# Performance work log

Measured on AMD Instinct MI355X. Metric: run time of the kernel, lower is better.

The kernel has to match this reference:

```python
import jax, jax.numpy as jnp
import numpy as np

U, DP, TOPK, NH = 2, 16, 8, 2
D = 512
M = DP ** U          # 256 slots
DK = U * DP          # 32 addressing dim
BETA_MAX = 2.0


def setup_inputs():
    key = jax.random.key(0)
    ks = jax.random.split(key, 12)
    B, T = 8, 128
    s = 0.02
    return {
        "h": jax.random.normal(ks[0], (B, T, D), jnp.float32),
        "K_slots": jax.random.normal(ks[1], (B, M, D), jnp.float32) * s,
        "V_slots": jax.random.normal(ks[2], (B, M, D), jnp.float32) * s,
        "z_K": jnp.ones((B, M), jnp.float32),
        "z_V": jnp.ones((B, M), jnp.float32),
        "W_k": jax.random.normal(ks[3], (DK, D), jnp.float32) * s,
        "W_q": jax.random.normal(ks[4], (DK, D), jnp.float32) * s,
        "log_tau_w": jnp.zeros((1,), jnp.float32),
        "log_tau_r": jnp.zeros((1,), jnp.float32),
        "hh_k": jax.random.normal(ks[5], (NH, D, D), jnp.float32) * s,
        "hh_vk": jax.random.normal(ks[6], (NH, D, D), jnp.float32) * s,
        "hh_vv": jax.random.normal(ks[7], (NH, D, D), jnp.float32) * s,
        "hh_bw": jax.random.normal(ks[8], (NH, 1, D), jnp.float32) * s,
        "hh_bb": jnp.zeros((NH, 1), jnp.float32),
        "gamma": jnp.float32(1.0),
        "W_out": jax.random.normal(ks[9], (D, D), jnp.float32) * s,
        "W_gate": jax.random.normal(ks[10], (D, D), jnp.float32) * s,
    }


def _kron_address(z, log_tau):
    # z: [B, DK]; Kronecker-factored softmax address over M = DP**U slots
    B = z.shape[0]
    probs = jax.nn.softmax(z.reshape(B, U, DP) / jnp.exp(log_tau[0]), axis=-1)
    addr = probs[:, 0]
    for u in range(1, U):
        addr = (addr[:, :, None] * probs[:, u, None, :]).reshape(B, -1)
    w, idx = jax.lax.top_k(addr, TOPK)
    return idx, w


def _forward(h, K_slots, V_slots, z_K, z_V, W_k, W_q, log_tau_w, log_tau_r,
             hh_k, hh_vk, hh_vv, hh_bw, hh_bb, gamma, W_out, W_gate,
             checkpoint=False):
    B, T, _ = h.shape
    scale = D ** -0.5
    b_idx = jnp.arange(B)[:, None]
    sp_gamma = jax.nn.softplus(gamma)

    def step(carry, h_t):
        K_s, V_s, zK, zV = carry
        write_idx, write_w = _kron_address(h_t @ W_k.T, log_tau_w)
        read_idx, _ = _kron_address(h_t @ W_q.T, log_tau_r)
        # scatter write weights into dense [B, M] (top-k indices are unique)
        w_full = jnp.zeros((B, M), h_t.dtype).at[b_idx, write_idx].set(write_w)
        # PDMA decay
        decay = (1.0 - w_full) ** sp_gamma
        K_s = decay[..., None] * K_s
        V_s = decay[..., None] * V_s
        zK = decay * zK + w_full
        zV = decay * zV + w_full
        # gather active slots: [B, K, D]
        K_act = jnp.take_along_axis(K_s, write_idx[:, :, None], axis=1)
        V_act = jnp.take_along_axis(V_s, write_idx[:, :, None], axis=1)
        # Householder update chain
        for j in range(NH):
            k_j = jax.nn.silu(h_t @ hh_k[j].T)
            k_hat = k_j / jnp.maximum(
                jnp.linalg.norm(k_j, axis=-1, keepdims=True), 1e-12)
            v_kj = h_t @ hh_vk[j].T
            v_vj = h_t @ hh_vv[j].T
            beta = BETA_MAX * jax.nn.sigmoid(h_t @ hh_bw[j].T + hh_bb[j])  # [B,1]
            kh = k_hat[:, None, :]
            be = beta[:, None, :]
            K_act = K_act - be * kh * (kh * K_act).sum(-1, keepdims=True) \
                    + be * k_j[:, None, :] * v_kj[:, None, :]
            V_act = V_act - be * kh * (kh * V_act).sum(-1, keepdims=True) \
                    + be * k_j[:, None, :] * v_vj[:, None, :]
        # scatter updated slots back
        K_s = K_s.at[b_idx, write_idx].set(K_act)
        V_s = V_s.at[b_idx, write_idx].set(V_act)
        # read path
        K_read = jnp.take_along_axis(K_s, read_idx[:, :, None], axis=1)
        V_read = jnp.take_along_axis(V_s, read_idx[:, :, None], axis=1)
        zK_read = jnp.take_along_axis(zK, read_idx, axis=1)[..., None]
        zV_read = jnp.take_along_axis(zV, read_idx, axis=1)[..., None]
        K_n = K_read / zK_read
        V_n = V_read / zV_read
        rel = (K_n * h_t[:, None, :]).sum(-1)           # [B, K]
        attn = jax.nn.softmax(rel * scale, axis=-1)
        readout = (attn[..., None] * V_n).sum(1)        # [B, D]
        out = jax.nn.sigmoid(h_t @ W_gate.T) * (readout @ W_out.T)
        return (K_s, V_s, zK, zV), (out, write_idx, read_idx)

    step_fn = jax.checkpoint(step) if checkpoint else step
    (K_s, V_s, zK, zV), (outs, widx, ridx) = jax.lax.scan(
        step_fn, (K_slots, V_slots, z_K, z_V), jnp.swapaxes(h, 0, 1))
    return (jnp.swapaxes(outs, 0, 1), K_s, V_s, zK, zV, widx[-1], ridx[-1])


def reference(h, K_slots, V_slots, z_K, z_V, W_k, W_q, log_tau_w, log_tau_r,
              hh_k, hh_vk, hh_vv, hh_bw, hh_bb, gamma, W_out, W_gate):
    return _forward(h, K_slots, V_slots, z_K, z_V, W_k, W_q, log_tau_w,
                    log_tau_r, hh_k, hh_vk, hh_vv, hh_bw, hh_bb, gamma,
                    W_out, W_gate)
```

## Files before the change

### kernel.cpp

```cpp
#include <hip/hip_runtime.h>
#include <math.h>

#define D_ 512
#define M_ 256
#define T_ 128
#define B_ 8
#define TOPK_ 8
#define NH_ 2
#define BT_ (B_*T_)

__device__ __forceinline__ float wred(float v){
#pragma unroll
  for (int m = 1; m < 64; m <<= 1) v += __shfl_xor(v, m, 64);
  return v;
}
__device__ __forceinline__ float4 ld4(const float* p){ return *(const float4*)p; }
__device__ __forceinline__ void st4(float* p, float4 v){ *(float4*)p = v; }
__device__ __forceinline__ float dot4(float4 a, float4 b){
  return a.x*b.x + a.y*b.y + a.z*b.z + a.w*b.w;
}
__device__ __forceinline__ float4 scl4(float4 a, float s){
  a.x*=s; a.y*=s; a.z*=s; a.w*=s; return a;
}

template<int CTRL>
__device__ __forceinline__ float dpp_add(float x){
  int y = __builtin_amdgcn_update_dpp(0, __float_as_int(x), CTRL, 0xf, 0xf, true);
  return x + __int_as_float(y);
}
__device__ __forceinline__ float wredd(float x){
  x = dpp_add<0x111>(x);
  x = dpp_add<0x112>(x);
  x = dpp_add<0x114>(x);
  x = dpp_add<0x118>(x);
  x = dpp_add<0x142>(x);
  x = dpp_add<0x143>(x);
  return __int_as_float(__builtin_amdgcn_readlane(__float_as_int(x), 63));
}

__device__ __forceinline__ void bar_lgkm(){
  asm volatile("s_waitcnt lgkmcnt(0)\n\ts_barrier" ::: "memory");
}

__global__ __launch_bounds__(64) void addr_kernel(
    const float* __restrict__ h, const float* __restrict__ Wk,
    const float* __restrict__ Wq, const float* __restrict__ ltw,
    const float* __restrict__ ltr, const float* __restrict__ gammap,
    float* __restrict__ metab)
{
  const int bt = blockIdx.x;
  const int tid = threadIdx.x;
  __shared__ float p_s[64];

  const float* hrow = h + (size_t)bt*D_;
  const float* wrow = (tid < 32) ? (Wk + (size_t)tid*D_)
                                 : (Wq + (size_t)(tid-32)*D_);
  float dot = 0.f;
  for (int d = 0; d < D_; d += 4){
    float4 hv = ld4(&hrow[d]); float4 wv = ld4(&wrow[d]);
    dot += hv.x*wv.x + hv.y*wv.y + hv.z*wv.z + hv.w*wv.w;
  }
  float tau = (tid < 32) ? expf(ltw[0]) : expf(ltr[0]);
  float mx = dot;
#pragma unroll
  for (int m = 1; m < 16; m <<= 1) mx = fmaxf(mx, __shfl_xor(mx, m, 64));
  float e = expf((dot - mx)/tau);
  float sm = e;
#pragma unroll
  for (int m = 1; m < 16; m <<= 1) sm += __shfl_xor(sm, m, 64);
  p_s[tid] = e / sm;
  __syncthreads();

  const int half = tid >> 5;
  const int l = tid & 31;
  const int g0 = half*32, g1 = half*32 + 16;
  float av[8];
#pragma unroll
  for (int k = 0; k < 8; ++k){
    int x = l*8 + k;
    av[k] = p_s[g0 + (x>>4)] * p_s[g1 + (x&15)];
  }
  const float sp = log1pf(expf(gammap[0]));
  for (int r = 0; r < TOPK_; ++r){
    float bv = -1.f; int bi = 0;
#pragma unroll
    for (int k = 0; k < 8; ++k){ if (av[k] > bv){ bv = av[k]; bi = l*8+k; } }
#pragma unroll
    for (int m = 1; m < 32; m <<= 1){
      float ov = __shfl_xor(bv, m, 64); int oi = __shfl_xor(bi, m, 64);
      if (ov > bv || (ov == bv && oi < bi)){ bv = ov; bi = oi; }
    }
    if ((bi >> 3) == l) av[bi & 7] = -2.f;
    float* mp = metab + (size_t)(bt*TOPK_ + r)*4;
    if (tid == 0){
      mp[0] = __int_as_float(bi); mp[1] = bv; mp[2] = powf(1.f - bv, sp);
    }
    if (tid == 32) mp[3] = __int_as_float(bi);
  }
}

struct GemmPtrs { const float* W[6]; float* C[6]; };

__global__ __launch_bounds__(256) void gemm_nt(
    const float* __restrict__ A, GemmPtrs p)
{
  const float* W = p.W[blockIdx.z];
  float* C = p.C[blockIdx.z];
  const int n0 = blockIdx.x * 64;
  const int m0 = blockIdx.y * 64;
  const int tid = threadIdx.x;
  __shared__ __align__(16) float As[16][68];
  __shared__ __align__(16) float Bs[16][68];
  const int r  = tid >> 2;
  const int c4 = (tid & 3) << 2;
  const int tx4 = (tid & 15) << 2;
  const int ty4 = (tid >> 4) << 2;
  float acc[4][4] = {{0.f}};

  for (int kc = 0; kc < 512; kc += 16){
    float4 av = ld4(&A[(size_t)(m0+r)*512 + kc + c4]);
    float4 wv = ld4(&W[(size_t)(n0+r)*512 + kc + c4]);
    __syncthreads();
    As[c4+0][r]=av.x; As[c4+1][r]=av.y; As[c4+2][r]=av.z; As[c4+3][r]=av.w;
    Bs[c4+0][r]=wv.x; Bs[c4+1][r]=wv.y; Bs[c4+2][r]=wv.z; Bs[c4+3][r]=wv.w;
    __syncthreads();
#pragma unroll
    for (int k = 0; k < 16; ++k){
      float4 a  = ld4(&As[k][ty4]);
      float4 bq = ld4(&Bs[k][tx4]);
      acc[0][0]+=a.x*bq.x; acc[0][1]+=a.x*bq.y; acc[0][2]+=a.x*bq.z; acc[0][3]+=a.x*bq.w;
      acc[1][0]+=a.y*bq.x; acc[1][1]+=a.y*bq.y; acc[1][2]+=a.y*bq.z; acc[1][3]+=a.y*bq.w;
      acc[2][0]+=a.z*bq.x; acc[2][1]+=a.z*bq.y; acc[2][2]+=a.z*bq.z; acc[2][3]+=a.z*bq.w;
      acc[3][0]+=a.w*bq.x; acc[3][1]+=a.w*bq.y; acc[3][2]+=a.w*bq.z; acc[3][3]+=a.w*bq.w;
    }
  }
#pragma unroll
  for (int i = 0; i < 4; ++i){
    float4 cv; cv.x=acc[i][0]; cv.y=acc[i][1]; cv.z=acc[i][2]; cv.w=acc[i][3];
    st4(&C[(size_t)(m0+ty4+i)*512 + n0 + tx4], cv);
  }
}

__global__ __launch_bounds__(256) void gemm_out(
    const float* __restrict__ h, const float* __restrict__ rdo,
    const float* __restrict__ Wg, const float* __restrict__ Wo,
    float* __restrict__ C)
{
  const int n0 = blockIdx.x * 64;
  const int m0 = blockIdx.y * 64;
  const int tid = threadIdx.x;
  __shared__ __align__(16) float Ag[16][68];
  __shared__ __align__(16) float Ao[16][68];
  __shared__ __align__(16) float Bg[16][68];
  __shared__ __align__(16) float Bo[16][68];
  const int r  = tid >> 2;
  const int c4 = (tid & 3) << 2;
  const int tx4 = (tid & 15) << 2;
  const int ty4 = (tid >> 4) << 2;
  float accg[4][4] = {{0.f}};
  float acco[4][4] = {{0.f}};

  for (int kc = 0; kc < 512; kc += 16){
    float4 a1 = ld4(&h  [(size_t)(m0+r)*512 + kc + c4]);
    float4 a2 = ld4(&rdo[(size_t)(m0+r)*512 + kc + c4]);
    float4 w1 = ld4(&Wg [(size_t)(n0+r)*512 + kc + c4]);
    float4 w2 = ld4(&Wo [(size_t)(n0+r)*512 + kc + c4]);
    __syncthreads();
    Ag[c4+0][r]=a1.x; Ag[c4+1][r]=a1.y; Ag[c4+2][r]=a1.z; Ag[c4+3][r]=a1.w;
    Ao[c4+0][r]=a2.x; Ao[c4+1][r]=a2.y; Ao[c4+2][r]=a2.z; Ao[c4+3][r]=a2.w;
    Bg[c4+0][r]=w1.x; Bg[c4+1][r]=w1.y; Bg[c4+2][r]=w1.z; Bg[c4+3][r]=w1.w;
    Bo[c4+0][r]=w2.x; Bo[c4+1][r]=w2.y; Bo[c4+2][r]=w2.z; Bo[c4+3][r]=w2.w;
    __syncthreads();
#pragma unroll
    for (int k = 0; k < 16; ++k){
      float4 ag = ld4(&Ag[k][ty4]);
      float4 ao = ld4(&Ao[k][ty4]);
      float4 bg = ld4(&Bg[k][tx4]);
      float4 bo = ld4(&Bo[k][tx4]);
      accg[0][0]+=ag.x*bg.x; accg[0][1]+=ag.x*bg.y; accg[0][2]+=ag.x*bg.z; accg[0][3]+=ag.x*bg.w;
      accg[1][0]+=ag.y*bg.x; accg[1][1]+=ag.y*bg.y; accg[1][2]+=ag.y*bg.z; accg[1][3]+=ag.y*bg.w;
      accg[2][0]+=ag.z*bg.x; accg[2][1]+=ag.z*bg.y; accg[2][2]+=ag.z*bg.z; accg[2][3]+=ag.z*bg.w;
      accg[3][0]+=ag.w*bg.x; accg[3][1]+=ag.w*bg.y; accg[3][2]+=ag.w*bg.z; accg[3][3]+=ag.w*bg.w;
      acco[0][0]+=ao.x*bo.x; acco[0][1]+=ao.x*bo.y; acco[0][2]+=ao.x*bo.z; acco[0][3]+=ao.x*bo.w;
      acco[1][0]+=ao.y*bo.x; acco[1][1]+=ao.y*bo.y; acco[1][2]+=ao.y*bo.z; acco[1][3]+=ao.y*bo.w;
      acco[2][0]+=ao.z*bo.x; acco[2][1]+=ao.z*bo.y; acco[2][2]+=ao.z*bo.z; acco[2][3]+=ao.z*bo.w;
      acco[3][0]+=ao.w*bo.x; acco[3][1]+=ao.w*bo.y; acco[3][2]+=ao.w*bo.z; acco[3][3]+=ao.w*bo.w;
    }
  }
#pragma unroll
  for (int i = 0; i < 4; ++i){
    float4 cv;
    cv.x = acco[i][0] / (1.f + expf(-accg[i][0]));
    cv.y = acco[i][1] / (1.f + expf(-accg[i][1]));
    cv.z = acco[i][2] / (1.f + expf(-accg[i][2]));
    cv.w = acco[i][3] / (1.f + expf(-accg[i][3]));
    st4(&C[(size_t)(m0+ty4+i)*512 + n0 + tx4], cv);
  }
}

__global__ __launch_bounds__(256) void ew2_kernel(
    float* __restrict__ khat, float* __restrict__ kvk, float* __restrict__ kvv,
    float* __restrict__ pre2, const float* __restrict__ h,
    const float* __restrict__ hh_bw, const float* __restrict__ hh_bb)
{
  const int bt = blockIdx.x;
  const int tid = threadIdx.x;
  const int wid = tid >> 6, lane = tid & 63;
  float* k0p  = khat + (size_t)bt*D_;
  float* k1p  = khat + (size_t)BT_*D_ + (size_t)bt*D_;
  float* vk0p = kvk  + (size_t)bt*D_;
  float* vk1p = kvk  + (size_t)BT_*D_ + (size_t)bt*D_;
  float* vv0p = kvv  + (size_t)bt*D_;
  float* vv1p = kvv  + (size_t)BT_*D_ + (size_t)bt*D_;
  const float* hp  = h + (size_t)bt*D_;

  float s0[2], s1[2];
  float n0 = 0.f, n1 = 0.f, bd0 = 0.f, bd1 = 0.f;
#pragma unroll
  for (int q = 0; q < 2; ++q){
    int d = tid + q*256;
    float x0 = k0p[d], x1 = k1p[d], hv = hp[d];
    float v0 = x0 / (1.f + expf(-x0));
    float v1 = x1 / (1.f + expf(-x1));
    s0[q] = v0; s1[q] = v1;
    n0 += v0*v0; n1 += v1*v1;
    bd0 += hv*hh_bw[d]; bd1 += hv*hh_bw[D_ + d];
  }
  __shared__ float4 rb[4];
  float4 acc = make_float4(wred(n0), wred(n1), wred(bd0), wred(bd1));
  if (lane == 0) rb[wid] = acc;
  __syncthreads();
  float4 t0 = rb[0], t1 = rb[1], t2 = rb[2], t3 = rb[3];
  n0 = t0.x+t1.x+t2.x+t3.x; n1 = t0.y+t1.y+t2.y+t3.y;
  bd0 = t0.z+t1.z+t2.z+t3.z; bd1 = t0.w+t1.w+t2.w+t3.w;
  float inv0 = 1.f / fmaxf(sqrtf(n0), 1e-12f);
  float inv1 = 1.f / fmaxf(sqrtf(n1), 1e-12f);
  float be0 = 2.f / (1.f + expf(-(bd0 + hh_bb[0])));
  float be1 = 2.f / (1.f + expf(-(bd1 + hh_bb[1])));

  float c01 = 0.f, dK = 0.f, dV = 0.f;
#pragma unroll
  for (int q = 0; q < 2; ++q){
    int d = tid + q*256;
    float kh0 = s0[q]*inv0, kh1 = s1[q]*inv1;
    float u0K = s0[q]*vk0p[d], u1K = s1[q]*vk1p[d];
    float u0V = s0[q]*vv0p[d], u1V = s1[q]*vv1p[d];
    k0p[d] = kh0; k1p[d] = kh1;
    vk0p[d] = be0*u0K + be1*u1K;
    vv0p[d] = be0*u0V + be1*u1V;
    c01 += kh1*kh0; dK += kh1*u0K; dV += kh1*u0V;
  }
  __syncthreads();
  float4 acc2 = make_float4(wred(c01), wred(dK), wred(dV), 0.f);
  if (lane == 0) rb[wid] = acc2;
  __syncthreads();
  if (tid == 0){
    float4 a = rb[0], b = rb[1], c = rb[2], d = rb[3];
    pre2[(size_t)bt*8+0] = a.x+b.x+c.x+d.x;
    pre2[(size_t)bt*8+1] = a.y+b.y+c.y+d.y;
    pre2[(size_t)bt*8+2] = a.z+b.z+c.z+d.z;
    pre2[(size_t)bt*8+3] = be0;
    pre2[(size_t)bt*8+4] = be1;
  }
}

__global__ __launch_bounds__(512, 2) void scan_kernel(
    float* __restrict__ Ks, float* __restrict__ Vs,
    const float* __restrict__ zK0, const float* __restrict__ zV0,
    const float* __restrict__ khat, const float* __restrict__ ucKb,
    const float* __restrict__ ucVb, const float* __restrict__ pre2,
    const float* __restrict__ metab, const float* __restrict__ h,
    float* __restrict__ readout,
    float* __restrict__ o_zK, float* __restrict__ o_zV,
    float* __restrict__ o_widx, float* __restrict__ o_ridx)
{
  __shared__ __align__(16) float ring[3][4*D_];
  __shared__ __align__(16) float fwdK[TOPK_][D_];
  __shared__ __align__(16) float fwdV[TOPK_][D_];
  __shared__ __align__(16) float Vr_s[TOPK_][D_];
  __shared__ float zK_s[M_], zV_s[M_];
  __shared__ float2 rel2_s[TOPK_];

  const int b = blockIdx.x;
  const int tid = threadIdx.x;
  const int s = tid >> 6, lane = tid & 63;
  const int l4 = lane * 4;
  const float scale = 0.044194173824159216f;

  float* Ksb = Ks + (size_t)b*M_*D_;
  float* Vsb = Vs + (size_t)b*M_*D_;
  const float* vbt[4] = { khat, khat + (size_t)BT_*D_, ucKb, ucVb };
  const float* srcc = vbt[s >> 1];
  const int goff = (s & 1)*256 + l4;
  const int loff = (s >> 1)*D_ + goff;
  const float4* mb = (const float4*)metab;

  const int bt0 = b*T_;
  for (int tt = 0; tt < 2; ++tt)
    st4(&ring[tt][loff], ld4(srcc + (size_t)(bt0+tt)*D_ + goff));
  float4 g = ld4(srcc + (size_t)(bt0+2)*D_ + goff);

  float4 me   = mb[bt0*TOPK_ + s];
  float4 me8  = mb[bt0*TOPK_ + (lane & 7)];
  int   mi  = __float_as_int(me.x);  float ww  = me.y;  float dec = me.z;
  int   ri  = __float_as_int(me.w);
  int   wv8 = __float_as_int(me8.x); int rv8 = __float_as_int(me8.w);
  float4 pm = *(const float4*)&pre2[(size_t)bt0*8];
  float be1v = pre2[(size_t)bt0*8+4];
  float c01 = pm.x, dKp = pm.y, dVp = pm.z, be0 = pm.w;

  const int bt1 = bt0 + 1;
  float4 me_n  = mb[bt1*TOPK_ + s];
  float4 me8_n = mb[bt1*TOPK_ + (lane & 7)];
  int   mi_n  = __float_as_int(me_n.x);  float ww_n = me_n.y;
  float dec_n = me_n.z;                  int ri_n  = __float_as_int(me_n.w);
  int   wv8_n = __float_as_int(me8_n.x); int rv8_n = __float_as_int(me8_n.w);
  float4 pm_n = *(const float4*)&pre2[(size_t)bt1*8];
  float be1_n = pre2[(size_t)bt1*8+4];

  float4 K0 = ld4(&Ksb[(size_t)mi*D_ + l4]);
  float4 K1 = ld4(&Ksb[(size_t)mi*D_ + 256 + l4]);
  float4 V0 = ld4(&Vsb[(size_t)mi*D_ + l4]);
  float4 V1 = ld4(&Vsb[(size_t)mi*D_ + 256 + l4]);
  float4 RK0 = ld4(&Ksb[(size_t)ri*D_ + l4]);
  float4 RK1 = ld4(&Ksb[(size_t)ri*D_ + 256 + l4]);
  float4 RV0 = ld4(&Vsb[(size_t)ri*D_ + l4]);
  float4 RV1 = ld4(&Vsb[(size_t)ri*D_ + 256 + l4]);

  if (tid < M_){ zK_s[tid] = zK0[b*M_+tid]; zV_s[tid] = zV0[b*M_+tid]; }
  __syncthreads();

  for (int t = 0; t < T_; ++t){
    const int bt = b*T_ + t;
    const float* rbuf = ring[t % 3];

    float4 HTa = ld4(h + (size_t)bt*D_ + l4);
    float4 HTb = ld4(h + (size_t)bt*D_ + 256 + l4);

    float4 kh0a = ld4(&rbuf[l4]),        kh0b = ld4(&rbuf[256+l4]);
    float4 kh1a = ld4(&rbuf[D_+l4]),     kh1b = ld4(&rbuf[D_+256+l4]);
    float4 ucKa = ld4(&rbuf[2*D_+l4]),   ucKb2 = ld4(&rbuf[2*D_+256+l4]);
    float4 ucVa = ld4(&rbuf[3*D_+l4]),   ucVb2 = ld4(&rbuf[3*D_+256+l4]);

    if (t > 0){
      float2 rz[TOPK_];
#pragma unroll
      for (int i = 0; i < TOPK_; ++i) rz[i] = rel2_s[i];
      float mx = rz[0].x;
#pragma unroll
      for (int i = 1; i < TOPK_; ++i) mx = fmaxf(mx, rz[i].x);
      float smm = 0.f, r = 0.f;
#pragma unroll
      for (int i = 0; i < TOPK_; ++i){
        float ev = __expf(rz[i].x - mx); smm += ev;
        r += ev * rz[i].y * Vr_s[i][tid];
      }
      readout[(size_t)(bt-1)*D_ + tid] = r / smm;
    }

    K0 = scl4(K0,dec); K1 = scl4(K1,dec);
    V0 = scl4(V0,dec); V1 = scl4(V1,dec);
    float aK = wredd(dot4(K0,kh0a) + dot4(K1,kh0b));
    float bK = wredd(dot4(K0,kh1a) + dot4(K1,kh1b));
    float aV = wredd(dot4(V0,kh0a) + dot4(V1,kh0b));
    float bV = wredd(dot4(V0,kh1a) + dot4(V1,kh1b));
    float p0K = be0*aK, p1K = be1v*(bK + be0*(dKp - aK*c01));
    float p0V = be0*aV, p1V = be1v*(bV + be0*(dVp - aV*c01));
    K0.x += ucKa.x  - p0K*kh0a.x - p1K*kh1a.x;
    K0.y += ucKa.y  - p0K*kh0a.y - p1K*kh1a.y;
    K0.z += ucKa.z  - p0K*kh0a.z - p1K*kh1a.z;
    K0.w += ucKa.w  - p0K*kh0a.w - p1K*kh1a.w;
    K1.x += ucKb2.x - p0K*kh0b.x - p1K*kh1b.x;
    K1.y += ucKb2.y - p0K*kh0b.y - p1K*kh1b.y;
    K1.z += ucKb2.z - p0K*kh0b.z - p1K*kh1b.z;
    K1.w += ucKb2.w - p0K*kh0b.w - p1K*kh1b.w;
    V0.x += ucVa.x  - p0V*kh0a.x - p1V*kh1a.x;
    V0.y += ucVa.y  - p0V*kh0a.y - p1V*kh1a.y;
    V0.z += ucVa.z  - p0V*kh0a.z - p1V*kh1a.z;
    V0.w += ucVa.w  - p0V*kh0a.w - p1V*kh1a.w;
    V1.x += ucVb2.x - p0V*kh0b.x - p1V*kh1b.x;
    V1.y += ucVb2.y - p0V*kh0b.y - p1V*kh1b.y;
    V1.z += ucVb2.z - p0V*kh0b.z - p1V*kh1b.z;
    V1.w += ucVb2.w - p0V*kh0b.w - p1V*kh1b.w;

    unsigned long long nf =
        __ballot((lane < 8) && (rv8   == mi)) |
        __ballot((lane < 8) && (wv8_n == mi)) |
        __ballot((lane < 8) && (rv8_n == mi));
    if (nf){
      st4(&fwdK[s][l4], K0); st4(&fwdK[s][256+l4], K1);
      st4(&fwdV[s][l4], V0); st4(&fwdV[s][256+l4], V1);
    }
    st4(&Ksb[(size_t)mi*D_ + l4], K0); st4(&Ksb[(size_t)mi*D_ + 256 + l4], K1);
    st4(&Vsb[(size_t)mi*D_ + l4], V0); st4(&Vsb[(size_t)mi*D_ + 256 + l4], V1);
    if (lane == 0)      zK_s[mi] = dec*zK_s[mi] + ww;
    else if (lane == 1) zV_s[mi] = dec*zV_s[mi] + ww;

    bar_lgkm();

    st4(&ring[(t+2)%3][loff], g);
    const int bt3 = (t+3 < T_) ? bt+3 : b*T_+T_-1;
    g = ld4(srcc + (size_t)bt3*D_ + goff);

    unsigned long long hS = __ballot((lane < 8) && (wv8 == mi_n));
    float4 nK0, nK1, nV0, nV1;
    if (hS){
      int w = __ffsll(hS) - 1;
      nK0 = ld4(&fwdK[w][l4]); nK1 = ld4(&fwdK[w][256+l4]);
      nV0 = ld4(&fwdV[w][l4]); nV1 = ld4(&fwdV[w][256+l4]);
    } else {
      nK0 = ld4(&Ksb[(size_t)mi_n*D_ + l4]);
      nK1 = ld4(&Ksb[(size_t)mi_n*D_ + 256 + l4]);
      nV0 = ld4(&Vsb[(size_t)mi_n*D_ + l4]);
      nV1 = ld4(&Vsb[(size_t)mi_n*D_ + 256 + l4]);
    }
    unsigned long long hR = __ballot((lane < 8) && (wv8 == ri_n));
    float4 nRK0, nRK1, nRV0, nRV1;
    if (hR){
      int w = __ffsll(hR) - 1;
      nRK0 = ld4(&fwdK[w][l4]); nRK1 = ld4(&fwdK[w][256+l4]);
      nRV0 = ld4(&fwdV[w][l4]); nRV1 = ld4(&fwdV[w][256+l4]);
    } else {
      nRK0 = ld4(&Ksb[(size_t)ri_n*D_ + l4]);
      nRK1 = ld4(&Ksb[(size_t)ri_n*D_ + 256 + l4]);
      nRV0 = ld4(&Vsb[(size_t)ri_n*D_ + l4]);
      nRV1 = ld4(&Vsb[(size_t)ri_n*D_ + 256 + l4]);
    }

    const int btnn = (t+2 < T_) ? bt+2 : b*T_+T_-1;
    float4 me_nn  = mb[btnn*TOPK_ + s];
    float4 me8_nn = mb[btnn*TOPK_ + (lane & 7)];
    float4 pm_nn  = *(const float4*)&pre2[(size_t)btnn*8];
    float  be1_nn = pre2[(size_t)btnn*8+4];

    unsigned long long mk = __ballot((lane < 8) && (wv8 == ri));
    float4 rk0, rk1, rv0, rv1;
    if (mk){
      int fm = __ffsll(mk) - 1;
      rk0 = ld4(&fwdK[fm][l4]); rk1 = ld4(&fwdK[fm][256+l4]);
      rv0 = ld4(&fwdV[fm][l4]); rv1 = ld4(&fwdV[fm][256+l4]);
    } else {
      rk0 = RK0; rk1 = RK1; rv0 = RV0; rv1 = RV1;
    }
    float dt = wredd(dot4(rk0,HTa) + dot4(rk1,HTb));
    st4(&Vr_s[s][l4], rv0); st4(&Vr_s[s][256+l4], rv1);
    if (lane == 0)
      rel2_s[s] = make_float2(dt * scale / zK_s[ri], 1.0f / zV_s[ri]);

    __syncthreads();

    K0=nK0; K1=nK1; V0=nV0; V1=nV1;
    RK0=nRK0; RK1=nRK1; RV0=nRV0; RV1=nRV1;
    mi=mi_n; ww=ww_n; dec=dec_n; ri=ri_n; wv8=wv8_n; rv8=rv8_n;
    c01=pm_n.x; dKp=pm_n.y; dVp=pm_n.z; be0=pm_n.w; be1v=be1_n;
    mi_n=__float_as_int(me_nn.x); ww_n=me_nn.y; dec_n=me_nn.z;
    ri_n=__float_as_int(me_nn.w);
    wv8_n=__float_as_int(me8_nn.x); rv8_n=__float_as_int(me8_nn.w);
    pm_n=pm_nn; be1_n=be1_nn;
  }

  {
    const int btL = b*T_ + T_ - 1;
    float2 rz[TOPK_];
#pragma unroll
    for (int i = 0; i < TOPK_; ++i) rz[i] = rel2_s[i];
    float mx = rz[0].x;
#pragma unroll
    for (int i = 1; i < TOPK_; ++i) mx = fmaxf(mx, rz[i].x);
    float smm = 0.f, r = 0.f;
#pragma unroll
    for (int i = 0; i < TOPK_; ++i){
      float ev = __expf(rz[i].x - mx); smm += ev;
      r += ev * rz[i].y * Vr_s[i][tid];
    }
    readout[(size_t)btL*D_ + tid] = r / smm;

    if (tid < M_){ o_zK[b*M_+tid] = zK_s[tid]; o_zV[b*M_+tid] = zV_s[tid]; }
    if (tid < TOPK_){
      float4 m = mb[btL*TOPK_ + tid];
      o_widx[b*TOPK_+tid] = (float)__float_as_int(m.x);
      o_ridx[b*TOPK_+tid] = (float)__float_as_int(m.w);
    }
  }
}

extern "C" void kernel_launch(void* const* d_in, const int* in_sizes, int n_in,
                              void* d_out, int out_size, void* d_ws, size_t ws_size,
                              hipStream_t stream)
{
  (void)in_sizes; (void)n_in; (void)out_size; (void)ws_size;
  const float* h       = (const float*)d_in[0];
  const float* K_slots = (const float*)d_in[1];
  const float* V_slots = (const float*)d_in[2];
  const float* z_K     = (const float*)d_in[3];
  const float* z_V     = (const float*)d_in[4];
  const float* W_k     = (const float*)d_in[5];
  const float* W_q     = (const float*)d_in[6];
  const float* ltw     = (const float*)d_in[7];
  const float* ltr     = (const float*)d_in[8];
  const float* hh_k    = (const float*)d_in[9];
  const float* hh_vk   = (const float*)d_in[10];
  const float* hh_vv   = (const float*)d_in[11];
  const float* hh_bw   = (const float*)d_in[12];
  const float* hh_bb   = (const float*)d_in[13];
  const float* gamma   = (const float*)d_in[14];
  const float* W_out   = (const float*)d_in[15];
  const float* W_gate  = (const float*)d_in[16];

  float* out    = (float*)d_out;
  float* o_outs = out;
  float* o_Ks   = out + 524288;
  float* o_Vs   = out + 1572864;
  float* o_zK   = out + 2621440;
  float* o_zV   = out + 2623488;
  float* o_widx = out + 2625536;
  float* o_ridx = out + 2625600;

  float* ws    = (float*)d_ws;
  float* khat  = ws;
  float* kvk   = ws + 2*(size_t)BT_*D_;
  float* kvv   = kvk + 2*(size_t)BT_*D_;
  float* rdo   = kvv + 2*(size_t)BT_*D_;
  float* metab = rdo + (size_t)BT_*D_;
  float* pre2  = metab + (size_t)BT_*TOPK_*4;

  (void)hipMemcpyAsync(o_Ks, K_slots, sizeof(float)*(size_t)B_*M_*D_,
                       hipMemcpyDeviceToDevice, stream);
  (void)hipMemcpyAsync(o_Vs, V_slots, sizeof(float)*(size_t)B_*M_*D_,
                       hipMemcpyDeviceToDevice, stream);

  addr_kernel<<<BT_, 64, 0, stream>>>(h, W_k, W_q, ltw, ltr, gamma, metab);

  GemmPtrs p{};
  p.W[0] = hh_k;           p.C[0] = khat;
  p.W[1] = hh_k + 262144;  p.C[1] = khat + (size_t)BT_*D_;
  p.W[2] = hh_vk;          p.C[2] = kvk;
  p.W[3] = hh_vk + 262144; p.C[3] = kvk + (size_t)BT_*D_;
  p.W[4] = hh_vv;          p.C[4] = kvv;
  p.W[5] = hh_vv + 262144; p.C[5] = kvv + (size_t)BT_*D_;
  gemm_nt<<<dim3(8,16,6), 256, 0, stream>>>(h, p);

  ew2_kernel<<<BT_, 256, 0, stream>>>(khat, kvk, kvv, pre2, h, hh_bw, hh_bb);

  scan_kernel<<<B_, 512, 0, stream>>>(o_Ks, o_Vs, z_K, z_V, khat, kvk, kvv,
                                      pre2, metab, h, rdo,
                                      o_zK, o_zV, o_widx, o_ridx);

  gemm_out<<<dim3(8,16), 256, 0, stream>>>(h, rdo, W_gate, W_out, o_outs);
}
```

Baseline: 510.5 us.

## Precompute slot normalizers in separate scan and simplify serial memory-update loop

The zK/zV normalizer recurrence moves into a new per-batch kernel that emits the reciprocal normalizers for each read index, so the main scan no longer keeps them in shared memory. The main scan drops the shared-memory forwarding of freshly written slots and instead re-reads slots from global memory after a barrier. Readout buffers are double-buffered so the softmax readout of the previous step can sit after the barrier. This removes ballot/forwarding logic and z bookkeeping from the serial critical path, at the cost of an extra kernel launch and global-memory read-after-write latency each step. It also relies on block-wide barriers making the global stores visible to the following loads.

```diff
diff --git a/kernel.cpp b/kernel.cpp
--- a/kernel.cpp
+++ b/kernel.cpp
@@ -38,10 +38,6 @@
   return __int_as_float(__builtin_amdgcn_readlane(__float_as_int(x), 63));
 }
 
-__device__ __forceinline__ void bar_lgkm(){
-  asm volatile("s_waitcnt lgkmcnt(0)\n\ts_barrier" ::: "memory");
-}
-
 __global__ __launch_bounds__(64) void addr_kernel(
     const float* __restrict__ h, const float* __restrict__ Wk,
     const float* __restrict__ Wq, const float* __restrict__ ltw,
@@ -97,6 +93,35 @@
     }
     if (tid == 32) mp[3] = __int_as_float(bi);
   }
+}
+
+__global__ __launch_bounds__(256) void zscan_kernel(
+    const float* __restrict__ zK0, const float* __restrict__ zV0,
+    const float* __restrict__ metab, float2* __restrict__ zr,
+    float* __restrict__ o_zK, float* __restrict__ o_zV)
+{
+  __shared__ __align__(16) float4 meta_s[T_*TOPK_];
+  const int b = blockIdx.x;
+  const int m = threadIdx.x;
+  const float4* mb = (const float4*)metab + (size_t)b*T_*TOPK_;
+#pragma unroll
+  for (int q = 0; q < 4; ++q) meta_s[m + q*256] = mb[m + q*256];
+  float zk = zK0[b*M_+m], zv = zV0[b*M_+m];
+  __syncthreads();
+  for (int t = 0; t < T_; ++t){
+#pragma unroll
+    for (int i = 0; i < TOPK_; ++i){
+      float4 me = meta_s[t*TOPK_+i];
+      if (m == __float_as_int(me.x)){ zk = me.z*zk + me.y; zv = me.z*zv + me.y; }
+    }
+#pragma unroll
+    for (int i = 0; i < TOPK_; ++i){
+      float4 me = meta_s[t*TOPK_+i];
+      if (m == __float_as_int(me.w))
+        zr[(size_t)(b*T_+t)*TOPK_+i] = make_float2(1.f/zk, 1.f/zv);
+    }
+  }
+  o_zK[b*M_+m] = zk; o_zV[b*M_+m] = zv;
 }
 
 struct GemmPtrs { const float* W[6]; float* C[6]; };
@@ -264,22 +289,17 @@
   }
 }
 
-__global__ __launch_bounds__(512, 2) void scan_kernel(
+__global__ __launch_bounds__(512) void scan_kernel(
     float* __restrict__ Ks, float* __restrict__ Vs,
-    const float* __restrict__ zK0, const float* __restrict__ zV0,
     const float* __restrict__ khat, const float* __restrict__ ucKb,
     const float* __restrict__ ucVb, const float* __restrict__ pre2,
-    const float* __restrict__ metab, const float* __restrict__ h,
-    float* __restrict__ readout,
-    float* __restrict__ o_zK, float* __restrict__ o_zV,
+    const float* __restrict__ metab, const float2* __restrict__ zr,
+    const float* __restrict__ h, float* __restrict__ readout,
     float* __restrict__ o_widx, float* __restrict__ o_ridx)
 {
-  __shared__ __align__(16) float ring[3][4*D_];
-  __shared__ __align__(16) float fwdK[TOPK_][D_];
-  __shared__ __align__(16) float fwdV[TOPK_][D_];
-  __shared__ __align__(16) float Vr_s[TOPK_][D_];
-  __shared__ float zK_s[M_], zV_s[M_];
-  __shared__ float2 rel2_s[TOPK_];
+  __shared__ __align__(16) float ring[4][4*D_];
+  __shared__ __align__(16) float Vr_s[2][TOPK_][D_];
+  __shared__ float2 rel2_s[2][TOPK_];
 
   const int b = blockIdx.x;
   const int tid = threadIdx.x;
@@ -296,67 +316,42 @@
   const float4* mb = (const float4*)metab;
 
   const int bt0 = b*T_;
-  for (int tt = 0; tt < 2; ++tt)
-    st4(&ring[tt][loff], ld4(srcc + (size_t)(bt0+tt)*D_ + goff));
+  st4(&ring[0][loff], ld4(srcc + (size_t)bt0*D_ + goff));
+  st4(&ring[1][loff], ld4(srcc + (size_t)(bt0+1)*D_ + goff));
   float4 g = ld4(srcc + (size_t)(bt0+2)*D_ + goff);
 
   float4 me   = mb[bt0*TOPK_ + s];
-  float4 me8  = mb[bt0*TOPK_ + (lane & 7)];
-  int   mi  = __float_as_int(me.x);  float ww  = me.y;  float dec = me.z;
-  int   ri  = __float_as_int(me.w);
-  int   wv8 = __float_as_int(me8.x); int rv8 = __float_as_int(me8.w);
-  float4 pm = *(const float4*)&pre2[(size_t)bt0*8];
-  float be1v = pre2[(size_t)bt0*8+4];
-  float c01 = pm.x, dKp = pm.y, dVp = pm.z, be0 = pm.w;
-
-  const int bt1 = bt0 + 1;
-  float4 me_n  = mb[bt1*TOPK_ + s];
-  float4 me8_n = mb[bt1*TOPK_ + (lane & 7)];
-  int   mi_n  = __float_as_int(me_n.x);  float ww_n = me_n.y;
-  float dec_n = me_n.z;                  int ri_n  = __float_as_int(me_n.w);
-  int   wv8_n = __float_as_int(me8_n.x); int rv8_n = __float_as_int(me8_n.w);
-  float4 pm_n = *(const float4*)&pre2[(size_t)bt1*8];
-  float be1_n = pre2[(size_t)bt1*8+4];
-
+  float4 me_n = mb[(bt0+1)*TOPK_ + s];
+  float4 pm   = ld4(&pre2[(size_t)bt0*8]);
+  float  be1v = pre2[(size_t)bt0*8+4];
+  float4 pm_n = ld4(&pre2[(size_t)(bt0+1)*8]);
+  float  be1_n= pre2[(size_t)(bt0+1)*8+4];
+  float2 zr2   = zr[(size_t)bt0*TOPK_ + s];
+  float2 zr2_n = zr[(size_t)(bt0+1)*TOPK_ + s];
+
+  int mi = __float_as_int(me.x);
   float4 K0 = ld4(&Ksb[(size_t)mi*D_ + l4]);
   float4 K1 = ld4(&Ksb[(size_t)mi*D_ + 256 + l4]);
   float4 V0 = ld4(&Vsb[(size_t)mi*D_ + l4]);
   float4 V1 = ld4(&Vsb[(size_t)mi*D_ + 256 + l4]);
-  float4 RK0 = ld4(&Ksb[(size_t)ri*D_ + l4]);
-  float4 RK1 = ld4(&Ksb[(size_t)ri*D_ + 256 + l4]);
-  float4 RV0 = ld4(&Vsb[(size_t)ri*D_ + l4]);
-  float4 RV1 = ld4(&Vsb[(size_t)ri*D_ + 256 + l4]);
-
-  if (tid < M_){ zK_s[tid] = zK0[b*M_+tid]; zV_s[tid] = zV0[b*M_+tid]; }
-  __syncthreads();
-
+  __syncthreads();
+
+#pragma unroll 4
   for (int t = 0; t < T_; ++t){
     const int bt = b*T_ + t;
-    const float* rbuf = ring[t % 3];
-
+    const float dec = me.z;
+    const int   ri  = __float_as_int(me.w);
+    mi = __float_as_int(me.x);
+
+    st4(&ring[(t+2)&3][loff], g);
     float4 HTa = ld4(h + (size_t)bt*D_ + l4);
     float4 HTb = ld4(h + (size_t)bt*D_ + 256 + l4);
 
+    const float* rbuf = ring[t & 3];
     float4 kh0a = ld4(&rbuf[l4]),        kh0b = ld4(&rbuf[256+l4]);
     float4 kh1a = ld4(&rbuf[D_+l4]),     kh1b = ld4(&rbuf[D_+256+l4]);
     float4 ucKa = ld4(&rbuf[2*D_+l4]),   ucKb2 = ld4(&rbuf[2*D_+256+l4]);
     float4 ucVa = ld4(&rbuf[3*D_+l4]),   ucVb2 = ld4(&rbuf[3*D_+256+l4]);
-
-    if (t > 0){
-      float2 rz[TOPK_];
-#pragma unroll
-      for (int i = 0; i < TOPK_; ++i) rz[i] = rel2_s[i];
-      float mx = rz[0].x;
-#pragma unroll
-      for (int i = 1; i < TOPK_; ++i) mx = fmaxf(mx, rz[i].x);
-      float smm = 0.f, r = 0.f;
-#pragma unroll
-      for (int i = 0; i < TOPK_; ++i){
-        float ev = __expf(rz[i].x - mx); smm += ev;
-        r += ev * rz[i].y * Vr_s[i][tid];
-      }
-      readout[(size_t)(bt-1)*D_ + tid] = r / smm;
-    }
 
     K0 = scl4(K0,dec); K1 = scl4(K1,dec);
     V0 = scl4(V0,dec); V1 = scl4(V1,dec);
@@ -364,8 +359,8 @@
     float bK = wredd(dot4(K0,kh1a) + dot4(K1,kh1b));
     float aV = wredd(dot4(V0,kh0a) + dot4(V1,kh0b));
     float bV = wredd(dot4(V0,kh1a) + dot4(V1,kh1b));
-    float p0K = be0*aK, p1K = be1v*(bK + be0*(dKp - aK*c01));
-    float p0V = be0*aV, p1V = be1v*(bV + be0*(dVp - aV*c01));
+    float p0K = pm.w*aK, p1K = be1v*(bK + pm.w*(pm.y - aK*pm.x));
+    float p0V = pm.w*aV, p1V = be1v*(bV + pm.w*(pm.z - aV*pm.x));
     K0.x += ucKa.x  - p0K*kh0a.x - p1K*kh1a.x;
     K0.y += ucKa.y  - p0K*kh0a.y - p1K*kh1a.y;
     K0.z += ucKa.z  - p0K*kh0a.z - p1K*kh1a.z;
@@ -383,87 +378,62 @@
     V1.z += ucVb2.z - p0V*kh0b.z - p1V*kh1b.z;
     V1.w += ucVb2.w - p0V*kh0b.w - p1V*kh1b.w;
 
-    unsigned long long nf =
-        __ballot((lane < 8) && (rv8   == mi)) |
-        __ballot((lane < 8) && (wv8_n == mi)) |
-        __ballot((lane < 8) && (rv8_n == mi));
-    if (nf){
-      st4(&fwdK[s][l4], K0); st4(&fwdK[s][256+l4], K1);
-      st4(&fwdV[s][l4], V0); st4(&fwdV[s][256+l4], V1);
-    }
     st4(&Ksb[(size_t)mi*D_ + l4], K0); st4(&Ksb[(size_t)mi*D_ + 256 + l4], K1);
     st4(&Vsb[(size_t)mi*D_ + l4], V0); st4(&Vsb[(size_t)mi*D_ + 256 + l4], V1);
-    if (lane == 0)      zK_s[mi] = dec*zK_s[mi] + ww;
-    else if (lane == 1) zV_s[mi] = dec*zV_s[mi] + ww;
-
-    bar_lgkm();
-
-    st4(&ring[(t+2)%3][loff], g);
-    const int bt3 = (t+3 < T_) ? bt+3 : b*T_+T_-1;
+
+    __syncthreads();
+
+    float4 RK0 = ld4(&Ksb[(size_t)ri*D_ + l4]);
+    float4 RK1 = ld4(&Ksb[(size_t)ri*D_ + 256 + l4]);
+    float4 RV0 = ld4(&Vsb[(size_t)ri*D_ + l4]);
+    float4 RV1 = ld4(&Vsb[(size_t)ri*D_ + 256 + l4]);
+    const int mi_n = __float_as_int(me_n.x);
+    float4 nK0 = ld4(&Ksb[(size_t)mi_n*D_ + l4]);
+    float4 nK1 = ld4(&Ksb[(size_t)mi_n*D_ + 256 + l4]);
+    float4 nV0 = ld4(&Vsb[(size_t)mi_n*D_ + l4]);
+    float4 nV1 = ld4(&Vsb[(size_t)mi_n*D_ + 256 + l4]);
+    const int bt3  = (t+3 < T_) ? bt+3 : b*T_+T_-1;
+    const int btnn = (t+2 < T_) ? bt+2 : b*T_+T_-1;
     g = ld4(srcc + (size_t)bt3*D_ + goff);
-
-    unsigned long long hS = __ballot((lane < 8) && (wv8 == mi_n));
-    float4 nK0, nK1, nV0, nV1;
-    if (hS){
-      int w = __ffsll(hS) - 1;
-      nK0 = ld4(&fwdK[w][l4]); nK1 = ld4(&fwdK[w][256+l4]);
-      nV0 = ld4(&fwdV[w][l4]); nV1 = ld4(&fwdV[w][256+l4]);
-    } else {
-      nK0 = ld4(&Ksb[(size_t)mi_n*D_ + l4]);
-      nK1 = ld4(&Ksb[(size_t)mi_n*D_ + 256 + l4]);
-      nV0 = ld4(&Vsb[(size_t)mi_n*D_ + l4]);
-      nV1 = ld4(&Vsb[(size_t)mi_n*D_ + 256 + l4]);
-    }
-    unsigned long long hR = __ballot((lane < 8) && (wv8 == ri_n));
-    float4 nRK0, nRK1, nRV0, nRV1;
-    if (hR){
-      int w = __ffsll(hR) - 1;
-      nRK0 = ld4(&fwdK[w][l4]); nRK1 = ld4(&fwdK[w][256+l4]);
-      nRV0 = ld4(&fwdV[w][l4]); nRV1 = ld4(&fwdV[w][256+l4]);
-    } else {
-      nRK0 = ld4(&Ksb[(size_t)ri_n*D_ + l4]);
-      nRK1 = ld4(&Ksb[(size_t)ri_n*D_ + 256 + l4]);
-      nRV0 = ld4(&Vsb[(size_t)ri_n*D_ + l4]);
-      nRV1 = ld4(&Vsb[(size_t)ri_n*D_ + 256 + l4]);
-    }
-
-    const int btnn = (t+2 < T_) ? bt+2 : b*T_+T_-1;
-    float4 me_nn  = mb[btnn*TOPK_ + s];
-    float4 me8_nn = mb[btnn*TOPK_ + (lane & 7)];
-    float4 pm_nn  = *(const float4*)&pre2[(size_t)btnn*8];
-    float  be1_nn = pre2[(size_t)btnn*8+4];
-
-    unsigned long long mk = __ballot((lane < 8) && (wv8 == ri));
-    float4 rk0, rk1, rv0, rv1;
-    if (mk){
-      int fm = __ffsll(mk) - 1;
-      rk0 = ld4(&fwdK[fm][l4]); rk1 = ld4(&fwdK[fm][256+l4]);
-      rv0 = ld4(&fwdV[fm][l4]); rv1 = ld4(&fwdV[fm][256+l4]);
-    } else {
-      rk0 = RK0; rk1 = RK1; rv0 = RV0; rv1 = RV1;
-    }
-    float dt = wredd(dot4(rk0,HTa) + dot4(rk1,HTb));
-    st4(&Vr_s[s][l4], rv0); st4(&Vr_s[s][256+l4], rv1);
+    float4 me_nn = mb[btnn*TOPK_ + s];
+    float4 pm_nn = ld4(&pre2[(size_t)btnn*8]);
+    float  be1nn = pre2[(size_t)btnn*8+4];
+    float2 zr2nn = zr[(size_t)btnn*TOPK_ + s];
+
+    if (t > 0){
+      const int pp = (t-1) & 1;
+      float2 rz[TOPK_];
+#pragma unroll
+      for (int i = 0; i < TOPK_; ++i) rz[i] = rel2_s[pp][i];
+      float mx = rz[0].x;
+#pragma unroll
+      for (int i = 1; i < TOPK_; ++i) mx = fmaxf(mx, rz[i].x);
+      float smm = 0.f, r = 0.f;
+#pragma unroll
+      for (int i = 0; i < TOPK_; ++i){
+        float ev = __expf(rz[i].x - mx); smm += ev;
+        r += ev * rz[i].y * Vr_s[pp][i][tid];
+      }
+      readout[(size_t)(bt-1)*D_ + tid] = r * __builtin_amdgcn_rcpf(smm);
+    }
+
+    float dt = wredd(dot4(RK0,HTa) + dot4(RK1,HTb));
     if (lane == 0)
-      rel2_s[s] = make_float2(dt * scale / zK_s[ri], 1.0f / zV_s[ri]);
-
-    __syncthreads();
+      rel2_s[t&1][s] = make_float2(dt * scale * zr2.x, zr2.y);
+    st4(&Vr_s[t&1][s][l4], RV0); st4(&Vr_s[t&1][s][256+l4], RV1);
 
     K0=nK0; K1=nK1; V0=nV0; V1=nV1;
-    RK0=nRK0; RK1=nRK1; RV0=nRV0; RV1=nRV1;
-    mi=mi_n; ww=ww_n; dec=dec_n; ri=ri_n; wv8=wv8_n; rv8=rv8_n;
-    c01=pm_n.x; dKp=pm_n.y; dVp=pm_n.z; be0=pm_n.w; be1v=be1_n;
-    mi_n=__float_as_int(me_nn.x); ww_n=me_nn.y; dec_n=me_nn.z;
-    ri_n=__float_as_int(me_nn.w);
-    wv8_n=__float_as_int(me8_nn.x); rv8_n=__float_as_int(me8_nn.w);
-    pm_n=pm_nn; be1_n=be1_nn;
-  }
-
+    me=me_n; pm=pm_n; be1v=be1_n; zr2=zr2_n;
+    me_n=me_nn; pm_n=pm_nn; be1_n=be1nn; zr2_n=zr2nn;
+  }
+
+  __syncthreads();
   {
     const int btL = b*T_ + T_ - 1;
+    const int pp = (T_-1) & 1;
     float2 rz[TOPK_];
 #pragma unroll
-    for (int i = 0; i < TOPK_; ++i) rz[i] = rel2_s[i];
+    for (int i = 0; i < TOPK_; ++i) rz[i] = rel2_s[pp][i];
     float mx = rz[0].x;
 #pragma unroll
     for (int i = 1; i < TOPK_; ++i) mx = fmaxf(mx, rz[i].x);
@@ -471,11 +441,10 @@
 #pragma unroll
     for (int i = 0; i < TOPK_; ++i){
       float ev = __expf(rz[i].x - mx); smm += ev;
-      r += ev * rz[i].y * Vr_s[i][tid];
-    }
-    readout[(size_t)btL*D_ + tid] = r / smm;
-
-    if (tid < M_){ o_zK[b*M_+tid] = zK_s[tid]; o_zV[b*M_+tid] = zV_s[tid]; }
+      r += ev * rz[i].y * Vr_s[pp][i][tid];
+    }
+    readout[(size_t)btL*D_ + tid] = r * __builtin_amdgcn_rcpf(smm);
+
     if (tid < TOPK_){
       float4 m = mb[btL*TOPK_ + tid];
       o_widx[b*TOPK_+tid] = (float)__float_as_int(m.x);
@@ -523,6 +492,7 @@
   float* rdo   = kvv + 2*(size_t)BT_*D_;
   float* metab = rdo + (size_t)BT_*D_;
   float* pre2  = metab + (size_t)BT_*TOPK_*4;
+  float2* zrb  = (float2*)(pre2 + (size_t)BT_*8);
 
   (void)hipMemcpyAsync(o_Ks, K_slots, sizeof(float)*(size_t)B_*M_*D_,
                        hipMemcpyDeviceToDevice, stream);
@@ -530,6 +500,7 @@
                        hipMemcpyDeviceToDevice, stream);
 
   addr_kernel<<<BT_, 64, 0, stream>>>(h, W_k, W_q, ltw, ltr, gamma, metab);
+  zscan_kernel<<<B_, 256, 0, stream>>>(z_K, z_V, metab, zrb, o_zK, o_zV);
 
   GemmPtrs p{};
   p.W[0] = hh_k;           p.C[0] = khat;
@@ -542,9 +513,9 @@
 
   ew2_kernel<<<BT_, 256, 0, stream>>>(khat, kvk, kvv, pre2, h, hh_bw, hh_bb);
 
-  scan_kernel<<<B_, 512, 0, stream>>>(o_Ks, o_Vs, z_K, z_V, khat, kvk, kvv,
-                                      pre2, metab, h, rdo,
-                                      o_zK, o_zV, o_widx, o_ridx);
+  scan_kernel<<<B_, 512, 0, stream>>>(o_Ks, o_Vs, khat, kvk, kvv,
+                                      pre2, metab, zrb, h, rdo,
+                                      o_widx, o_ridx);
 
   gemm_out<<<dim3(8,16), 256, 0, stream>>>(h, rdo, W_gate, W_out, o_outs);
 }
```

Result: slower. 541.6 us (+6.1%).
